# Kernel tuning notes

Hardware: AMD Instinct MI355X
Metric: run time of the kernel (lower is better)

The kernel has to match this reference:

```python
import jax, jax.numpy as jnp
import numpy as np

B, V, E = 32, 2048, 12288
IMG_F = 512
GCN_DIMS = [(3 + IMG_F, 512), (512, 512), (512, 512), (512, 512), (512, 64), (64, 3)]
FC_DIMS = [(V * 3, 1024), (1024, 1024), (1024, V * 3)]


def setup_inputs() -> dict:
    key = jax.random.key(0)
    ks = jax.random.split(key, 3 + len(GCN_DIMS) + len(FC_DIMS))
    inp = {}
    inp["vertices"] = jax.random.normal(ks[0], (B, V, 3), dtype=jnp.float32)
    inp["img_features"] = jax.random.normal(ks[1], (B, IMG_F), dtype=jnp.float32)
    inp["edge_index"] = jax.random.randint(ks[2], (2, E), 0, V, dtype=jnp.int32)
    for i, (fi, fo) in enumerate(GCN_DIMS):
        inp[f"W{i+1}"] = (jax.random.normal(ks[3 + i], (fi, fo), dtype=jnp.float32) / np.sqrt(fi)).astype(jnp.float32)
        inp[f"b{i+1}"] = jnp.zeros((fo,), dtype=jnp.float32)
    for i, (fi, fo) in enumerate(FC_DIMS):
        inp[f"fcW{i+1}"] = (jax.random.normal(ks[3 + len(GCN_DIMS) + i], (fi, fo), dtype=jnp.float32) / np.sqrt(fi)).astype(jnp.float32)
        inp[f"fcb{i+1}"] = jnp.zeros((fo,), dtype=jnp.float32)
    return inp


def _gcn_norm(edge_index):
    # PyG GCNConv: add self-loops, symmetric normalization 1/sqrt(d_i d_j).
    loop = jnp.arange(V, dtype=edge_index.dtype)
    src = jnp.concatenate([edge_index[0], loop])
    dst = jnp.concatenate([edge_index[1], loop])
    deg = jax.ops.segment_sum(jnp.ones_like(dst, dtype=jnp.float32), dst, num_segments=V)
    dinv = jax.lax.rsqrt(deg)  # deg >= 1 due to self-loops
    norm = dinv[src] * dinv[dst]  # [E+V]
    return src, dst, norm


def _gcn_layer(x, W, b, src, dst, norm):
    # x: [B, V, Fin] -> [B, V, Fout]; transform then gather/scatter aggregate.
    h = jnp.einsum("bvi,io->bvo", x, W)
    msg = h[:, src, :] * norm[None, :, None]          # gather over edges
    agg = jax.vmap(lambda m: jax.ops.segment_sum(m, dst, num_segments=V))(msg)
    return agg + b


def reference(vertices, img_features, edge_index,
              W1, b1, W2, b2, W3, b3, W4, b4, W5, b5, W6, b6,
              fcW1, fcb1, fcW2, fcb2, fcW3, fcb3):
    src, dst, norm = _gcn_norm(edge_index)
    # concat vertex coords with broadcast image feature: [B, V, 3+512]
    x = jnp.concatenate([vertices, jnp.broadcast_to(img_features[:, None, :], (B, V, IMG_F))], axis=2)
    x = _gcn_layer(x, W1, b1, src, dst, norm)
    x = _gcn_layer(x, W2, b2, src, dst, norm)
    x = jax.nn.relu(x)
    x = _gcn_layer(x, W3, b3, src, dst, norm)
    x = _gcn_layer(x, W4, b4, src, dst, norm)
    x = jax.nn.relu(x)
    x = _gcn_layer(x, W5, b5, src, dst, norm)
    x = _gcn_layer(x, W6, b6, src, dst, norm)
    x = jax.nn.relu(x)
    x = x.reshape(B, V * 3)
    h = x @ fcW1 + fcb1
    h = h @ fcW2 + fcb2
    h = jnp.tanh(h @ fcW3 + fcb3)
    deformations = h.reshape(B, V, 3) * 0.1
    return vertices + deformations
```

## Files before the change

kernel.cpp:

```cpp
#include <hip/hip_runtime.h>
#include <stdint.h>
#include <math.h>

#define B_ 32
#define V_ 2048
#define E_ 12288
#define M_ (B_*V_)

typedef __bf16 bf16x8 __attribute__((ext_vector_type(8)));
typedef float f32x4 __attribute__((ext_vector_type(4)));

__device__ __forceinline__ float bf2f(unsigned short u){
  union { unsigned int i; float f; } v; v.i = ((unsigned int)u) << 16; return v.f;
}
__device__ __forceinline__ unsigned short f2bf(float f){
  union { float f; unsigned int i; } v; v.f = f;
  unsigned int r = (v.i + 0x7fffu + ((v.i >> 16) & 1u)) >> 16;
  return (unsigned short)r;
}
__device__ __forceinline__ void gload16(const unsigned short* g, unsigned short* l){
  __builtin_amdgcn_global_load_lds(
      (const __attribute__((address_space(1))) void*)g,
      (__attribute__((address_space(3))) void*)l, 16, 0, 0);
}

__global__ __launch_bounds__(1024) void k_pre0(
    const int* __restrict__ ei, int* __restrict__ rowptr_g, int* __restrict__ cols_g,
    float* __restrict__ vals_g, float* __restrict__ selfw_g,
    float* __restrict__ wsum_g, float* __restrict__ w2_g,
    const float* __restrict__ W3, const float* __restrict__ W4,
    const float* __restrict__ img, const float* __restrict__ W1,
    unsigned short* __restrict__ W3B, unsigned short* __restrict__ W4T,
    float* __restrict__ partB){
  __shared__ int   sdeg[V_];
  __shared__ int   srp[V_ + 1];
  __shared__ int   sfill[V_];
  __shared__ float sdinv[V_];
  __shared__ float swsum[V_];
  __shared__ float sw2[V_];
  __shared__ int   swt[16];
  __shared__ __align__(16) float tile[4][32][33];
  if (blockIdx.x == 0){
    const int t = threadIdx.x;
    sdeg[2*t] = 0; sdeg[2*t+1] = 0; sfill[2*t] = 0; sfill[2*t+1] = 0;
    __syncthreads();
    #pragma unroll
    for (int e = t; e < E_; e += 1024) atomicAdd(&sdeg[ei[E_ + e]], 1);
    __syncthreads();
    int c0 = sdeg[2*t], c1 = sdeg[2*t+1];
    int s2 = c0 + c1;
    int lane = t & 63, wid = t >> 6;
    int pre = s2;
    #pragma unroll
    for (int off = 1; off < 64; off <<= 1){
      int u = __shfl_up(pre, off);
      if (lane >= off) pre += u;
    }
    if (lane == 63) swt[wid] = pre;
    __syncthreads();
    if (t == 0){
      int run = 0;
      #pragma unroll
      for (int i = 0; i < 16; i++){ int x = swt[i]; swt[i] = run; run += x; }
      srp[V_] = run;
    }
    __syncthreads();
    int base = swt[wid] + (pre - s2);
    srp[2*t] = base; srp[2*t+1] = base + c0;
    #pragma unroll
    for (int v = t; v < V_; v += 1024){
      float d = (float)(sdeg[v] + 1);
      float di = rsqrtf(d);
      sdinv[v] = di;
      swsum[v] = di * di;
    }
    __syncthreads();
    #pragma unroll
    for (int e = t; e < E_; e += 1024){
      int s = ei[e], d = ei[E_ + e];
      int pos = srp[d] + atomicAdd(&sfill[d], 1);
      float val = sdinv[s] * sdinv[d];
      cols_g[pos] = s;
      vals_g[pos] = val;
      atomicAdd(&swsum[d], val);
    }
    __syncthreads();
    #pragma unroll
    for (int v = t; v < V_; v += 1024)
      sw2[v] = (sdinv[v] * sdinv[v]) * swsum[v];
    __syncthreads();
    #pragma unroll
    for (int e = t; e < E_; e += 1024){
      int s = ei[e], d = ei[E_ + e];
      atomicAdd(&sw2[d], sdinv[s] * sdinv[d] * swsum[s]);
    }
    __syncthreads();
    #pragma unroll
    for (int v = t; v < V_; v += 1024){
      rowptr_g[v] = srp[v];
      selfw_g[v]  = sdinv[v] * sdinv[v];
      wsum_g[v]   = swsum[v];
      w2_g[v]     = sw2[v];
    }
    if (t == 0) rowptr_g[V_] = srp[V_];
  } else {
    int u = blockIdx.x - 1;
    int t10 = threadIdx.x;
    int sub = (u << 2) + (t10 >> 8);
    int t = t10 & 255;
    int ti = t10 >> 8;
    if (sub < 256){
      int tr0 = (sub >> 4) << 5, tc0 = (sub & 15) << 5;
      int r = t >> 5, c = t & 31;
      #pragma unroll
      for (int i = 0; i < 4; i++)
        tile[ti][r + 8*i][c] = W4[(size_t)(tr0 + r + 8*i) * 512 + tc0 + c];
      __syncthreads();
      #pragma unroll
      for (int i = 0; i < 4; i++)
        W4T[(size_t)(tc0 + r + 8*i) * 512 + tr0 + c] = f2bf(tile[ti][c][r + 8*i]);
    } else if (sub < 256 + 1024){
      int id = (sub - 256) * 256 + t;
      W3B[id] = f2bf(W3[id]);
    } else {
      int g = sub - 1280;
      int kc = g >> 1, nh = g & 1;
      int k0 = kc * 16;
      float* xs = &tile[ti][0][0];
      for (int i = t; i < 512; i += 256)
        xs[i] = img[(size_t)(i >> 4) * 512 + k0 + (i & 15)];
      __syncthreads();
      const float* W = W1 + 3 * 512;
      int n = (nh << 8) + t;
      float acc[32] = {};
      #pragma unroll
      for (int kg = 0; kg < 4; kg++){
        const float* wp = W + (size_t)(k0 + kg * 4) * 512 + n;
        float w0 = wp[0], w1 = wp[512], w2 = wp[1024], w3 = wp[1536];
        #pragma unroll
        for (int r = 0; r < 32; r++){
          f32x4 xv = *(const f32x4*)&xs[r * 16 + kg * 4];
          acc[r] += xv[0]*w0 + xv[1]*w1 + xv[2]*w2 + xv[3]*w3;
        }
      }
      float* p = partB + (size_t)kc * 16384 + n;
      #pragma unroll
      for (int r = 0; r < 32; r++) p[(size_t)r * 512] = acc[r];
    }
  }
}

__global__ __launch_bounds__(256) void k_preB(
    const float* __restrict__ partB, float* __restrict__ I1,
    const float* __restrict__ b3, const float* __restrict__ W4,
    const float* __restrict__ W5, const float* __restrict__ W6,
    const float* __restrict__ b5,
    float* __restrict__ C34, float* __restrict__ W56, float* __restrict__ C56){
  int blk = blockIdx.x, t = threadIdx.x;
  if (blk < 64){
    int id = blk * 256 + t;
    float a = 0.f;
    #pragma unroll
    for (int s = 0; s < 32; s++) a += partB[(size_t)s * 16384 + id];
    I1[id] = a;
  } else {
    int id = (blk - 64) * 256 + t;
    if (id < 512){
      float a0=0,a1=0,a2=0,a3=0;
      for (int k = 0; k < 512; k += 4){
        a0 += b3[k]   * W4[(size_t)k * 512 + id];
        a1 += b3[k+1] * W4[(size_t)(k+1) * 512 + id];
        a2 += b3[k+2] * W4[(size_t)(k+2) * 512 + id];
        a3 += b3[k+3] * W4[(size_t)(k+3) * 512 + id];
      }
      C34[id] = a0+a1+a2+a3;
    } else if (id < 512 + 1536){
      int i = id - 512; int k5 = i / 3, j = i % 3;
      float a = 0.f;
      #pragma unroll 4
      for (int u = 0; u < 64; u++) a += W5[k5 * 64 + u] * W6[u * 3 + j];
      W56[i] = a;
    } else if (id < 512 + 1536 + 3){
      int j = id - (512 + 1536);
      float a = 0.f;
      #pragma unroll 4
      for (int u = 0; u < 64; u++) a += b5[u] * W6[u * 3 + j];
      C56[j] = a;
    }
  }
}

__global__ __launch_bounds__(256) void k_preC(
    const float* __restrict__ b1, const float* __restrict__ W1,
    const float* __restrict__ I1, const float* __restrict__ W2,
    float* __restrict__ partB){
  __shared__ __align__(16) float xs[36 * 16];
  int g = blockIdx.x;
  int kc = g >> 1, k0 = kc * 16;
  int t = threadIdx.x;
  int n = ((g & 1) << 8) + t;
  for (int i = t; i < 576; i += 256){
    int r = i >> 4, kk = i & 15;
    const float* q;
    if (r == 0)      q = b1;
    else if (r < 4)  q = W1 + (size_t)(r - 1) * 512;
    else             q = I1 + (size_t)(r - 4) * 512;
    xs[i] = q[k0 + kk];
  }
  __syncthreads();
  float acc[36] = {};
  #pragma unroll
  for (int kg = 0; kg < 4; kg++){
    const float* wp = W2 + (size_t)(k0 + kg * 4) * 512 + n;
    float w0 = wp[0], w1 = wp[512], w2 = wp[1024], w3 = wp[1536];
    #pragma unroll
    for (int r = 0; r < 36; r++){
      f32x4 xv = *(const f32x4*)&xs[r * 16 + kg * 4];
      acc[r] += xv[0]*w0 + xv[1]*w1 + xv[2]*w2 + xv[3]*w3;
    }
  }
  float* p = partB + (size_t)kc * 18432 + n;
  #pragma unroll
  for (int r = 0; r < 36; r++) p[(size_t)r * 512] = acc[r];
}

__global__ __launch_bounds__(256) void k_preD(
    const float* __restrict__ partB, float* __restrict__ P){
  int id = blockIdx.x * 256 + threadIdx.x;
  float a = 0.f;
  #pragma unroll
  for (int s = 0; s < 32; s++) a += partB[(size_t)s * 18432 + id];
  P[id] = a;
}

__global__ __launch_bounds__(1024) void k_va2(
    const float* __restrict__ in, const int* __restrict__ rowptr,
    const int* __restrict__ cols, const float* __restrict__ vals,
    const float* __restrict__ selfw, float* __restrict__ outv){
  __shared__ float xs[V_ * 3];
  __shared__ float ys[V_ * 3];
  int b = blockIdx.x, t = threadIdx.x;
  const float* ib = in + (size_t)b * V_ * 3;
  for (int i = t; i < V_ * 3; i += 1024) xs[i] = ib[i];
  __syncthreads();
  for (int v = t; v < V_; v += 1024){
    float sw = selfw[v];
    float a0 = sw * xs[v*3], a1 = sw * xs[v*3+1], a2 = sw * xs[v*3+2];
    int re = rowptr[v + 1];
    for (int e = rowptr[v]; e < re; e++){
      int s = cols[e]; float vv = vals[e];
      a0 += vv * xs[s*3]; a1 += vv * xs[s*3+1]; a2 += vv * xs[s*3+2];
    }
    ys[v*3] = a0; ys[v*3+1] = a1; ys[v*3+2] = a2;
  }
  __syncthreads();
  for (int v = t; v < V_; v += 1024){
    float sw = selfw[v];
    float a0 = sw * ys[v*3], a1 = sw * ys[v*3+1], a2 = sw * ys[v*3+2];
    int re = rowptr[v + 1];
    for (int e = rowptr[v]; e < re; e++){
      int s = cols[e]; float vv = vals[e];
      a0 += vv * ys[s*3]; a1 += vv * ys[s*3+1]; a2 += vv * ys[s*3+2];
    }
    float* o = outv + ((size_t)v * 32 + b) * 3;
    o[0] = a0; o[1] = a1; o[2] = a2;
  }
}

__global__ __launch_bounds__(1024) void k_x2(
    const float* __restrict__ va2v, const float* __restrict__ P,
    const float* __restrict__ wsum, const float* __restrict__ w2s,
    const float* __restrict__ b2,
    unsigned short* __restrict__ Y){
  int v = (blockIdx.x << 2) + (threadIdx.x >> 8);
  int batch = (blockIdx.y << 2) + ((threadIdx.x >> 6) & 3);
  int f8 = (threadIdx.x & 63) * 8;
  const float* va = va2v + ((size_t)v * 32 + batch) * 3;
  float x0 = va[0], x1 = va[1], x2 = va[2];
  float w2v = w2s[v], wsv = wsum[v];
  float tt[8];
  #pragma unroll
  for (int h = 0; h < 2; h++){
    f32x4 wv0 = *(const f32x4*)&P[512  + f8 + 4*h];
    f32x4 wv1 = *(const f32x4*)&P[1024 + f8 + 4*h];
    f32x4 wv2 = *(const f32x4*)&P[1536 + f8 + 4*h];
    f32x4 ccv = *(const f32x4*)&P[f8 + 4*h];
    f32x4 bbv = *(const f32x4*)&b2[f8 + 4*h];
    f32x4 iiv = *(const f32x4*)&P[2048 + (size_t)batch * 512 + f8 + 4*h];
    #pragma unroll
    for (int j = 0; j < 4; j++){
      float tv = x0*wv0[j] + x1*wv1[j] + x2*wv2[j] + w2v*iiv[j] + wsv*ccv[j] + bbv[j];
      tt[4*h + j] = fmaxf(tv, 0.f);
    }
  }
  unsigned int o[4];
  #pragma unroll
  for (int i = 0; i < 4; i++)
    o[i] = (unsigned int)f2bf(tt[2*i]) | ((unsigned int)f2bf(tt[2*i+1]) << 16);
  *(uint4*)&Y[((size_t)v * 32 + batch) * 512 + f8] = *(uint4*)o;
}

__global__ __launch_bounds__(128) void k_aggv(
    const unsigned short* __restrict__ Hg, const int* __restrict__ rowptr,
    const int* __restrict__ cols, const float* __restrict__ vals,
    const float* __restrict__ selfw, unsigned short* __restrict__ Xo){
  int bid = blockIdx.x;
  int bg  = bid & 7;
  int dst = (bid >> 3) & (V_ - 1);
  int fc  = bid >> 14;
  int t = threadIdx.x;
  int batch = (bg << 2) + (t >> 5);
  int f8 = (fc << 8) + (t & 31) * 8;
  int rs = rowptr[dst], re = rowptr[dst + 1];
  float sw = selfw[dst];
  float a[8];
  {
    uint4 q = *(const uint4*)&Hg[((size_t)dst * 32 + batch) * 512 + f8];
    const unsigned int* w = (const unsigned int*)&q;
    #pragma unroll
    for (int i = 0; i < 4; i++){
      a[2*i]   = sw * bf2f(w[i] & 0xffff);
      a[2*i+1] = sw * bf2f(w[i] >> 16);
    }
  }
  int e = rs;
  for (; e + 1 < re; e += 2){
    int s0 = cols[e], s1 = cols[e+1];
    float v0 = vals[e], v1 = vals[e+1];
    uint4 q0 = *(const uint4*)&Hg[((size_t)s0 * 32 + batch) * 512 + f8];
    uint4 q1 = *(const uint4*)&Hg[((size_t)s1 * 32 + batch) * 512 + f8];
    const unsigned int* w0 = (const unsigned int*)&q0;
    const unsigned int* w1 = (const unsigned int*)&q1;
    #pragma unroll
    for (int i = 0; i < 4; i++){
      a[2*i]   += v0 * bf2f(w0[i] & 0xffff) + v1 * bf2f(w1[i] & 0xffff);
      a[2*i+1] += v0 * bf2f(w0[i] >> 16)    + v1 * bf2f(w1[i] >> 16);
    }
  }
  if (e < re){
    int s = cols[e]; float v = vals[e];
    uint4 q = *(const uint4*)&Hg[((size_t)s * 32 + batch) * 512 + f8];
    const unsigned int* w = (const unsigned int*)&q;
    #pragma unroll
    for (int i = 0; i < 4; i++){
      a[2*i]   += v * bf2f(w[i] & 0xffff);
      a[2*i+1] += v * bf2f(w[i] >> 16);
    }
  }
  unsigned int o[4];
  #pragma unroll
  for (int i = 0; i < 4; i++)
    o[i] = (unsigned int)f2bf(a[2*i]) | ((unsigned int)f2bf(a[2*i+1]) << 16);
  *(uint4*)&Xo[((size_t)dst * 32 + batch) * 512 + f8] = *(uint4*)o;
}

template<int BM, int BN, int WM, int WN, int TM, int TN>
__global__ __launch_bounds__(WM*WN*64) void k_gemm(
    const unsigned short* __restrict__ Xg, const unsigned short* __restrict__ Wt,
    unsigned short* __restrict__ Hg, int K, int N,
    const float* __restrict__ wsumv, const float* __restrict__ cvec,
    const float* __restrict__ bias, int relu,
    const float* __restrict__ W56g, float* __restrict__ h5p){
  constexpr int BK = 32;
  constexpr int NW = WM * WN;
  constexpr int NT = NW * 64;
  constexpr int RA = BM / NW;
  constexpr int RB = BN / NW;
  __shared__ __align__(16) unsigned short As[2][BM * BK];
  __shared__ __align__(16) unsigned short Bs[2][BN * BK];
  __shared__ float h5s[BM * 3];
  const int tid = threadIdx.x;
  const int row0 = blockIdx.x * BM, col0 = blockIdx.y * BN;
  const int wave = tid >> 6, lane = tid & 63;
  const int wr = wave / WN, wc = wave % WN;
  const int lrow = lane & 15, lq = lane >> 4;
  const int lrw = lane >> 2, lcol = (lane & 3) * 8;
  const int arow = wave * RA, brow = wave * RB;
  if (h5p){
    for (int i = tid; i < BM * 3; i += NT) h5s[i] = 0.f;
  }
  f32x4 acc[TM][TN] = {};
  #pragma unroll
  for (int t = 0; t < RA / 16; t++)
    gload16(&Xg[(size_t)(row0 + arow + t * 16 + lrw) * K + lcol],
            &As[0][(arow + t * 16) * BK]);
  #pragma unroll
  for (int t = 0; t < RB / 16; t++)
    gload16(&Wt[(size_t)(col0 + brow + t * 16 + lrw) * K + lcol],
            &Bs[0][(brow + t * 16) * BK]);
  int cur = 0;
  for (int k0 = 0; k0 < K; k0 += BK){
    __syncthreads();
    if (k0 + BK < K){
      #pragma unroll
      for (int t = 0; t < RA / 16; t++)
        gload16(&Xg[(size_t)(row0 + arow + t * 16 + lrw) * K + k0 + BK + lcol],
                &As[cur ^ 1][(arow + t * 16) * BK]);
      #pragma unroll
      for (int t = 0; t < RB / 16; t++)
        gload16(&Wt[(size_t)(col0 + brow + t * 16 + lrw) * K + k0 + BK + lcol],
                &Bs[cur ^ 1][(brow + t * 16) * BK]);
    }
    bf16x8 af[TM], bfr[TN];
    #pragma unroll
    for (int tm = 0; tm < TM; tm++)
      af[tm] = *(const bf16x8*)&As[cur][(wr * TM * 16 + tm * 16 + lrow) * BK + lq * 8];
    #pragma unroll
    for (int tn = 0; tn < TN; tn++)
      bfr[tn] = *(const bf16x8*)&Bs[cur][(wc * TN * 16 + tn * 16 + lrow) * BK + lq * 8];
    #pragma unroll
    for (int tm = 0; tm < TM; tm++)
      #pragma unroll
      for (int tn = 0; tn < TN; tn++)
        acc[tm][tn] = __builtin_amdgcn_mfma_f32_16x16x32_bf16(af[tm], bfr[tn], acc[tm][tn], 0, 0, 0);
    cur ^= 1;
  }
  if (h5p){
    float w56l[TN][3], cvl[TN], bvl[TN];
    #pragma unroll
    for (int tn = 0; tn < TN; tn++){
      int col = col0 + wc * TN * 16 + tn * 16 + lrow;
      cvl[tn] = cvec[col]; bvl[tn] = bias[col];
      w56l[tn][0] = W56g[col * 3];
      w56l[tn][1] = W56g[col * 3 + 1];
      w56l[tn][2] = W56g[col * 3 + 2];
    }
    #pragma unroll
    for (int tm = 0; tm < TM; tm++){
      #pragma unroll
      for (int r = 0; r < 4; r++){
        int lr = wr * TM * 16 + tm * 16 + lq * 4 + r;
        float ws = wsumv[(row0 + lr) >> 5];
        float p0 = 0.f, p1 = 0.f, p2 = 0.f;
        #pragma unroll
        for (int tn = 0; tn < TN; tn++){
          float x = fmaxf(acc[tm][tn][r] + ws * cvl[tn] + bvl[tn], 0.f);
          p0 += x * w56l[tn][0]; p1 += x * w56l[tn][1]; p2 += x * w56l[tn][2];
        }
        #pragma unroll
        for (int off = 8; off; off >>= 1){
          p0 += __shfl_down(p0, off);
          p1 += __shfl_down(p1, off);
          p2 += __shfl_down(p2, off);
        }
        if (lrow == 0){
          atomicAdd(&h5s[lr * 3 + 0], p0);
          atomicAdd(&h5s[lr * 3 + 1], p1);
          atomicAdd(&h5s[lr * 3 + 2], p2);
        }
      }
    }
    __syncthreads();
    float* dst = h5p + (size_t)blockIdx.y * ((size_t)M_ * 3) + (size_t)row0 * 3;
    for (int i = tid; i < BM * 3; i += NT) dst[i] = h5s[i];
  } else {
    #pragma unroll
    for (int tm = 0; tm < TM; tm++){
      #pragma unroll
      for (int tn = 0; tn < TN; tn++){
        int col = col0 + wc * TN * 16 + tn * 16 + lrow;
        float cv = 0.f, bv = 0.f;
        if (cvec){ cv = cvec[col]; bv = bias[col]; }
        #pragma unroll
        for (int r = 0; r < 4; r++){
          int row = row0 + wr * TM * 16 + tm * 16 + lq * 4 + r;
          float x = acc[tm][tn][r];
          if (cvec) x += wsumv[row >> 5] * cv + bv;
          if (relu) x = fmaxf(x, 0.f);
          Hg[(size_t)row * N + col] = f2bf(x);
        }
      }
    }
  }
}

__global__ __launch_bounds__(1024) void k_xa2(
    const float* __restrict__ h5p, const int* __restrict__ rowptr,
    const int* __restrict__ cols, const float* __restrict__ vals,
    const float* __restrict__ selfw, const float* __restrict__ wsum,
    const float* __restrict__ C56, const float* __restrict__ b6,
    float* __restrict__ XF){
  __shared__ float xs[V_ * 3];
  __shared__ float ys[V_ * 3];
  int b = blockIdx.x, t = threadIdx.x;
  const size_t M3 = (size_t)M_ * 3;
  for (int i = t; i < V_ * 3; i += 1024){
    int v = i / 3, j = i - v * 3;
    size_t g = ((size_t)v * 32 + b) * 3 + j;
    xs[i] = h5p[g] + h5p[M3 + g] + h5p[2 * M3 + g] + h5p[3 * M3 + g];
  }
  __syncthreads();
  for (int v = t; v < V_; v += 1024){
    float sw = selfw[v];
    float a0 = sw * xs[v*3], a1 = sw * xs[v*3+1], a2 = sw * xs[v*3+2];
    int re = rowptr[v + 1];
    for (int e = rowptr[v]; e < re; e++){
      int s = cols[e]; float vv = vals[e];
      a0 += vv * xs[s*3]; a1 += vv * xs[s*3+1]; a2 += vv * xs[s*3+2];
    }
    ys[v*3] = a0; ys[v*3+1] = a1; ys[v*3+2] = a2;
  }
  __syncthreads();
  float* ob = XF + (size_t)b * V_ * 3;
  for (int v = t; v < V_; v += 1024){
    float sw = selfw[v];
    float a0 = sw * ys[v*3], a1 = sw * ys[v*3+1], a2 = sw * ys[v*3+2];
    int re = rowptr[v + 1];
    for (int e = rowptr[v]; e < re; e++){
      int s = cols[e]; float vv = vals[e];
      a0 += vv * ys[s*3]; a1 += vv * ys[s*3+1]; a2 += vv * ys[s*3+2];
    }
    float w = wsum[v];
    a0 = fmaxf(a0 + w * C56[0] + b6[0], 0.f);
    a1 = fmaxf(a1 + w * C56[1] + b6[1], 0.f);
    a2 = fmaxf(a2 + w * C56[2] + b6[2], 0.f);
    ob[v*3] = a0; ob[v*3+1] = a1; ob[v*3+2] = a2;
  }
}

template<int R, int KC>
__global__ __launch_bounds__(256) void k_fcp(
    const float* __restrict__ in, const float* __restrict__ W,
    float* __restrict__ partial, int K, int N){
  const int n = blockIdx.x * 256 + threadIdx.x;
  const int k0 = blockIdx.y * KC;
  float acc[R] = {};
  for (int kk = 0; kk < KC; kk += 4){
    const float* wp = W + (size_t)(k0 + kk) * N + n;
    float w0 = wp[0];
    float w1 = wp[(size_t)N];
    float w2 = wp[(size_t)2 * N];
    float w3 = wp[(size_t)3 * N];
    #pragma unroll
    for (int r = 0; r < R; r++){
      const float* xp = in + (size_t)r * K + k0 + kk;
      acc[r] += xp[0]*w0 + xp[1]*w1 + xp[2]*w2 + xp[3]*w3;
    }
  }
  float* p = partial + (size_t)blockIdx.y * R * N + n;
  #pragma unroll
  for (int r = 0; r < R; r++) p[(size_t)r * N] = acc[r];
}

__global__ __launch_bounds__(256) void k_fcr(
    const float* __restrict__ partial, const float* __restrict__ bias,
    float* __restrict__ out, int total, int N, int KS, int mode,
    const float* __restrict__ vert){
  int id = blockIdx.x * 256 + threadIdx.x;
  if (id >= total) return;
  int n = id % N;
  float a0 = 0.f, a1 = 0.f, a2 = 0.f, a3 = 0.f;
  int s = 0;
  for (; s + 4 <= KS; s += 4){
    a0 += partial[(size_t)s * total + id];
    a1 += partial[(size_t)(s + 1) * total + id];
    a2 += partial[(size_t)(s + 2) * total + id];
    a3 += partial[(size_t)(s + 3) * total + id];
  }
  for (; s < KS; s++) a0 += partial[(size_t)s * total + id];
  float acc = a0 + a1 + a2 + a3;
  if (bias) acc += bias[n];
  if (mode) acc = vert[id] + 0.1f * tanhf(acc);
  out[id] = acc;
}

static constexpr size_t AL(size_t x){ return (x + 255) & ~(size_t)255; }
static constexpr size_t S512 = (size_t)M_ * 512 * 2;
static constexpr size_t S3   = (size_t)M_ * 3 * 4;
static constexpr size_t OXA  = 0;
static constexpr size_t OXB  = OXA  + AL(S512);
static constexpr size_t OVA2 = OXB  + AL(S512);
static constexpr size_t OH5P = OVA2 + AL(S3);
static constexpr size_t OXF  = OH5P + AL(4 * S3);
static constexpr size_t OFC1 = OXF  + AL(S3);
static constexpr size_t OFC2 = OFC1 + AL((size_t)B_ * 1024 * 4);
static constexpr size_t OI1  = OFC2 + AL((size_t)B_ * 1024 * 4);
static constexpr size_t OP   = OI1  + AL((size_t)32 * 512 * 4);
static constexpr size_t OC34 = OP   + AL((size_t)36 * 512 * 4);
static constexpr size_t OW56 = OC34 + AL((size_t)512 * 4);
static constexpr size_t OC56 = OW56 + AL((size_t)512 * 3 * 4);
static constexpr size_t OW3B = OC56 + AL((size_t)3 * 4);
static constexpr size_t OW4T = OW3B + AL((size_t)512 * 512 * 2);
static constexpr size_t OW34 = OW4T + AL((size_t)512 * 512 * 2);
static constexpr size_t OROW = OW34 + AL((size_t)512 * 512 * 2);
static constexpr size_t OCOL = OROW + AL((size_t)(V_ + 1) * 4);
static constexpr size_t OVAL = OCOL + AL((size_t)E_ * 4);
static constexpr size_t OSELF= OVAL + AL((size_t)E_ * 4);
static constexpr size_t OWS  = OSELF+ AL((size_t)V_ * 4);
static constexpr size_t OW2S = OWS  + AL((size_t)V_ * 4);

extern "C" void kernel_launch(void* const* d_in, const int* in_sizes, int n_in,
                              void* d_out, int out_size, void* d_ws, size_t ws_size,
                              hipStream_t stream){
  const float* vert  = (const float*)d_in[0];
  const float* img   = (const float*)d_in[1];
  const int*   ei    = (const int*)  d_in[2];
  const float* W1 = (const float*)d_in[3],  *b1 = (const float*)d_in[4];
  const float* W2 = (const float*)d_in[5],  *b2 = (const float*)d_in[6];
  const float* W3 = (const float*)d_in[7],  *b3 = (const float*)d_in[8];
  const float* W4 = (const float*)d_in[9],  *b4 = (const float*)d_in[10];
  const float* W5 = (const float*)d_in[11], *b5 = (const float*)d_in[12];
  const float* W6 = (const float*)d_in[13], *b6 = (const float*)d_in[14];
  const float* fcW1 = (const float*)d_in[15], *fcb1 = (const float*)d_in[16];
  const float* fcW2 = (const float*)d_in[17], *fcb2 = (const float*)d_in[18];
  const float* fcW3 = (const float*)d_in[19], *fcb3 = (const float*)d_in[20];
  float* out = (float*)d_out;

  char* ws = (char*)d_ws;
  unsigned short* XA  = (unsigned short*)(ws + OXA);
  unsigned short* XB  = (unsigned short*)(ws + OXB);
  float* VA2v = (float*)(ws + OVA2);
  float* H5P  = (float*)(ws + OH5P);
  float* XF   = (float*)(ws + OXF);
  float* FC1o = (float*)(ws + OFC1);
  float* FC2o = (float*)(ws + OFC2);
  float* I1   = (float*)(ws + OI1);
  float* P    = (float*)(ws + OP);
  float* C34  = (float*)(ws + OC34);
  float* W56  = (float*)(ws + OW56);
  float* C56  = (float*)(ws + OC56);
  unsigned short* W3B = (unsigned short*)(ws + OW3B);
  unsigned short* W4T = (unsigned short*)(ws + OW4T);
  unsigned short* W34 = (unsigned short*)(ws + OW34);
  float* PARTA = (float*)(ws + OXA);
  float* PARTB = (float*)(ws + OXB);
  int*   ROW  = (int*)(ws + OROW);
  int*   COL  = (int*)(ws + OCOL);
  float* VAL  = (float*)(ws + OVAL);
  float* SELF = (float*)(ws + OSELF);
  float* WSUM = (float*)(ws + OWS);
  float* W2S  = (float*)(ws + OW2S);

  k_pre0<<<337, 1024, 0, stream>>>(ei, ROW, COL, VAL, SELF, WSUM, W2S,
                                   W3, W4, img, W1, W3B, W4T, PARTB);
  k_preB<<<64 + 9, 256, 0, stream>>>(PARTB, I1, b3, W4, W5, W6, b5, C34, W56, C56);
  k_preC<<<64, 256, 0, stream>>>(b1, W1, I1, W2, PARTB);
  k_preD<<<72, 256, 0, stream>>>(PARTB, P);
  k_gemm<64,64,2,2,2,2><<<dim3(8, 8), 256, 0, stream>>>(W4T, W3B, W34, 512, 512,
                                                        nullptr, nullptr, nullptr, 0,
                                                        nullptr, nullptr);

  k_va2<<<B_, 1024, 0, stream>>>(vert, ROW, COL, VAL, SELF, VA2v);
  k_x2<<<dim3(V_ / 4, 8), 1024, 0, stream>>>(VA2v, P, WSUM, W2S, b2, XA);
  k_aggv<<<V_ * 16, 128, 0, stream>>>(XA, ROW, COL, VAL, SELF, XB);
  k_aggv<<<V_ * 16, 128, 0, stream>>>(XB, ROW, COL, VAL, SELF, XA);

  k_gemm<128,128,2,2,4,4><<<dim3(M_ / 128, 4), 256, 0, stream>>>(XA, W34, XB, 512, 512,
                                                                 WSUM, C34, b4, 1,
                                                                 W56, H5P);

  k_xa2<<<B_, 1024, 0, stream>>>(H5P, ROW, COL, VAL, SELF, WSUM, C56, b6, XF);

  k_fcp<32,64><<<dim3(4, 96), 256, 0, stream>>>(XF, fcW1, PARTA, 6144, 1024);
  k_fcr<<<(B_ * 1024 + 255) / 256, 256, 0, stream>>>(PARTA, fcb1, FC1o, 32 * 1024, 1024, 96, 0, nullptr);
  k_fcp<32,64><<<dim3(4, 16), 256, 0, stream>>>(FC1o, fcW2, PARTA, 1024, 1024);
  k_fcr<<<(B_ * 1024 + 255) / 256, 256, 0, stream>>>(PARTA, fcb2, FC2o, 32 * 1024, 1024, 16, 0, nullptr);
  k_fcp<32,64><<<dim3(24, 16), 256, 0, stream>>>(FC2o, fcW3, PARTA, 1024, 6144);
  k_fcr<<<(B_ * 6144 + 255) / 256, 256, 0, stream>>>(PARTA, fcb3, out, 32 * 6144, 6144, 16, 1, vert);
}
```

Before: 539.7 us.

## Loop N tiles inside GEMM block and regroup aggregation blocks by vertex

After: 559.9 us. 3.7% more time.

```diff
diff --git a/kernel.cpp b/kernel.cpp
--- a/kernel.cpp
+++ b/kernel.cpp
@@ -9,6 +9,7 @@
 
 typedef __bf16 bf16x8 __attribute__((ext_vector_type(8)));
 typedef float f32x4 __attribute__((ext_vector_type(4)));
+typedef unsigned int u32x4 __attribute__((ext_vector_type(4)));
 
 __device__ __forceinline__ float bf2f(unsigned short u){
   union { unsigned int i; float f; } v; v.i = ((unsigned int)u) << 16; return v.f;
@@ -300,17 +301,20 @@
   *(uint4*)&Y[((size_t)v * 32 + batch) * 512 + f8] = *(uint4*)o;
 }
 
-__global__ __launch_bounds__(128) void k_aggv(
+__global__ __launch_bounds__(256) void k_aggv(
     const unsigned short* __restrict__ Hg, const int* __restrict__ rowptr,
     const int* __restrict__ cols, const float* __restrict__ vals,
     const float* __restrict__ selfw, unsigned short* __restrict__ Xo){
   int bid = blockIdx.x;
-  int bg  = bid & 7;
-  int dst = (bid >> 3) & (V_ - 1);
-  int fc  = bid >> 14;
+  int bgLo = bid & 7;
+  int dstB = (bid >> 3) & 511;
+  int bgHi = (bid >> 12) & 1;
+  int fc   = bid >> 13;
   int t = threadIdx.x;
-  int batch = (bg << 2) + (t >> 5);
-  int f8 = (fc << 8) + (t & 31) * 8;
+  int wave = t >> 6, lane = t & 63;
+  int dst = dstB * 4 + wave;
+  int batch = bgHi * 16 + bgLo * 2 + (lane >> 5);
+  int f8 = fc * 256 + (lane & 31) * 8;
   int rs = rowptr[dst], re = rowptr[dst + 1];
   float sw = selfw[dst];
   float a[8];
@@ -347,14 +351,14 @@
       a[2*i+1] += v * bf2f(w[i] >> 16);
     }
   }
-  unsigned int o[4];
+  u32x4 o;
   #pragma unroll
   for (int i = 0; i < 4; i++)
     o[i] = (unsigned int)f2bf(a[2*i]) | ((unsigned int)f2bf(a[2*i+1]) << 16);
-  *(uint4*)&Xo[((size_t)dst * 32 + batch) * 512 + f8] = *(uint4*)o;
-}
-
-template<int BM, int BN, int WM, int WN, int TM, int TN>
+  __builtin_nontemporal_store(o, (u32x4*)&Xo[((size_t)dst * 32 + batch) * 512 + f8]);
+}
+
+template<int BM, int BN, int WM, int WN, int TM, int TN, int NL>
 __global__ __launch_bounds__(WM*WN*64) void k_gemm(
     const unsigned short* __restrict__ Xg, const unsigned short* __restrict__ Wt,
     unsigned short* __restrict__ Hg, int K, int N,
@@ -370,7 +374,8 @@
   __shared__ __align__(16) unsigned short Bs[2][BN * BK];
   __shared__ float h5s[BM * 3];
   const int tid = threadIdx.x;
-  const int row0 = blockIdx.x * BM, col0 = blockIdx.y * BN;
+  const int row0 = blockIdx.x * BM;
+  const int colB0 = blockIdx.y * BN * NL;
   const int wave = tid >> 6, lane = tid & 63;
   const int wr = wave / WN, wc = wave % WN;
   const int lrow = lane & 15, lq = lane >> 4;
@@ -386,91 +391,104 @@
             &As[0][(arow + t * 16) * BK]);
   #pragma unroll
   for (int t = 0; t < RB / 16; t++)
-    gload16(&Wt[(size_t)(col0 + brow + t * 16 + lrw) * K + lcol],
+    gload16(&Wt[(size_t)(colB0 + brow + t * 16 + lrw) * K + lcol],
             &Bs[0][(brow + t * 16) * BK]);
   int cur = 0;
-  for (int k0 = 0; k0 < K; k0 += BK){
-    __syncthreads();
-    if (k0 + BK < K){
-      #pragma unroll
-      for (int t = 0; t < RA / 16; t++)
-        gload16(&Xg[(size_t)(row0 + arow + t * 16 + lrw) * K + k0 + BK + lcol],
-                &As[cur ^ 1][(arow + t * 16) * BK]);
-      #pragma unroll
-      for (int t = 0; t < RB / 16; t++)
-        gload16(&Wt[(size_t)(col0 + brow + t * 16 + lrw) * K + k0 + BK + lcol],
-                &Bs[cur ^ 1][(brow + t * 16) * BK]);
-    }
-    bf16x8 af[TM], bfr[TN];
-    #pragma unroll
-    for (int tm = 0; tm < TM; tm++)
-      af[tm] = *(const bf16x8*)&As[cur][(wr * TM * 16 + tm * 16 + lrow) * BK + lq * 8];
-    #pragma unroll
-    for (int tn = 0; tn < TN; tn++)
-      bfr[tn] = *(const bf16x8*)&Bs[cur][(wc * TN * 16 + tn * 16 + lrow) * BK + lq * 8];
-    #pragma unroll
-    for (int tm = 0; tm < TM; tm++)
+  for (int nt = 0; nt < NL; nt++){
+    const int col0 = colB0 + nt * BN;
+    for (int k0 = 0; k0 < K; k0 += BK){
+      __syncthreads();
+      int k2 = k0 + BK, nt2 = nt;
+      if (k2 >= K){ k2 = 0; nt2 = nt + 1; }
+      if (nt2 < NL){
+        #pragma unroll
+        for (int t = 0; t < RA / 16; t++)
+          gload16(&Xg[(size_t)(row0 + arow + t * 16 + lrw) * K + k2 + lcol],
+                  &As[cur ^ 1][(arow + t * 16) * BK]);
+        #pragma unroll
+        for (int t = 0; t < RB / 16; t++)
+          gload16(&Wt[(size_t)(colB0 + nt2 * BN + brow + t * 16 + lrw) * K + k2 + lcol],
+                  &Bs[cur ^ 1][(brow + t * 16) * BK]);
+      }
+      bf16x8 af[TM], bfr[TN];
+      #pragma unroll
+      for (int tm = 0; tm < TM; tm++)
+        af[tm] = *(const bf16x8*)&As[cur][(wr * TM * 16 + tm * 16 + lrow) * BK + lq * 8];
       #pragma unroll
       for (int tn = 0; tn < TN; tn++)
-        acc[tm][tn] = __builtin_amdgcn_mfma_f32_16x16x32_bf16(af[tm], bfr[tn], acc[tm][tn], 0, 0, 0);
-    cur ^= 1;
-  }
-  if (h5p){
-    float w56l[TN][3], cvl[TN], bvl[TN];
-    #pragma unroll
-    for (int tn = 0; tn < TN; tn++){
-      int col = col0 + wc * TN * 16 + tn * 16 + lrow;
-      cvl[tn] = cvec[col]; bvl[tn] = bias[col];
-      w56l[tn][0] = W56g[col * 3];
-      w56l[tn][1] = W56g[col * 3 + 1];
-      w56l[tn][2] = W56g[col * 3 + 2];
-    }
-    #pragma unroll
-    for (int tm = 0; tm < TM; tm++){
-      #pragma unroll
-      for (int r = 0; r < 4; r++){
-        int lr = wr * TM * 16 + tm * 16 + lq * 4 + r;
-        float ws = wsumv[(row0 + lr) >> 5];
-        float p0 = 0.f, p1 = 0.f, p2 = 0.f;
+        bfr[tn] = *(const bf16x8*)&Bs[cur][(wc * TN * 16 + tn * 16 + lrow) * BK + lq * 8];
+      #pragma unroll
+      for (int tm = 0; tm < TM; tm++)
+        #pragma unroll
+        for (int tn = 0; tn < TN; tn++)
+          acc[tm][tn] = __builtin_amdgcn_mfma_f32_16x16x32_bf16(af[tm], bfr[tn], acc[tm][tn], 0, 0, 0);
+      cur ^= 1;
+    }
+    if (h5p){
+      float w56l[TN][3], cvl[TN], bvl[TN];
+      #pragma unroll
+      for (int tn = 0; tn < TN; tn++){
+        int col = col0 + wc * TN * 16 + tn * 16 + lrow;
+        cvl[tn] = cvec[col]; bvl[tn] = bias[col];
+        w56l[tn][0] = W56g[col * 3];
+        w56l[tn][1] = W56g[col * 3 + 1];
+        w56l[tn][2] = W56g[col * 3 + 2];
+      }
+      #pragma unroll
+      for (int tm = 0; tm < TM; tm++){
+        #pragma unroll
+        for (int r = 0; r < 4; r++){
+          int lr = wr * TM * 16 + tm * 16 + lq * 4 + r;
+          float ws = wsumv[(row0 + lr) >> 5];
+          float p0 = 0.f, p1 = 0.f, p2 = 0.f;
+          #pragma unroll
+          for (int tn = 0; tn < TN; tn++){
+            float x = fmaxf(acc[tm][tn][r] + ws * cvl[tn] + bvl[tn], 0.f);
+            p0 += x * w56l[tn][0]; p1 += x * w56l[tn][1]; p2 += x * w56l[tn][2];
+          }
+          #pragma unroll
+          for (int off = 8; off; off >>= 1){
+            p0 += __shfl_down(p0, off);
+            p1 += __shfl_down(p1, off);
+            p2 += __shfl_down(p2, off);
+          }
+          if (lrow == 0){
+            atomicAdd(&h5s[lr * 3 + 0], p0);
+            atomicAdd(&h5s[lr * 3 + 1], p1);
+            atomicAdd(&h5s[lr * 3 + 2], p2);
+          }
+        }
+      }
+      #pragma unroll
+      for (int tm = 0; tm < TM; tm++)
+        #pragma unroll
+        for (int tn = 0; tn < TN; tn++)
+          acc[tm][tn] = (f32x4){0.f, 0.f, 0.f, 0.f};
+    } else {
+      #pragma unroll
+      for (int tm = 0; tm < TM; tm++){
         #pragma unroll
         for (int tn = 0; tn < TN; tn++){
-          float x = fmaxf(acc[tm][tn][r] + ws * cvl[tn] + bvl[tn], 0.f);
-          p0 += x * w56l[tn][0]; p1 += x * w56l[tn][1]; p2 += x * w56l[tn][2];
-        }
-        #pragma unroll
-        for (int off = 8; off; off >>= 1){
-          p0 += __shfl_down(p0, off);
-          p1 += __shfl_down(p1, off);
-          p2 += __shfl_down(p2, off);
-        }
-        if (lrow == 0){
-          atomicAdd(&h5s[lr * 3 + 0], p0);
-          atomicAdd(&h5s[lr * 3 + 1], p1);
-          atomicAdd(&h5s[lr * 3 + 2], p2);
+          int col = col0 + wc * TN * 16 + tn * 16 + lrow;
+          float cv = 0.f, bv = 0.f;
+          if (cvec){ cv = cvec[col]; bv = bias[col]; }
+          #pragma unroll
+          for (int r = 0; r < 4; r++){
+            int row = row0 + wr * TM * 16 + tm * 16 + lq * 4 + r;
+            float x = acc[tm][tn][r];
+            if (cvec) x += wsumv[row >> 5] * cv + bv;
+            if (relu) x = fmaxf(x, 0.f);
+            Hg[(size_t)row * N + col] = f2bf(x);
+          }
+          acc[tm][tn] = (f32x4){0.f, 0.f, 0.f, 0.f};
         }
       }
     }
+  }
+  if (h5p){
     __syncthreads();
     float* dst = h5p + (size_t)blockIdx.y * ((size_t)M_ * 3) + (size_t)row0 * 3;
     for (int i = tid; i < BM * 3; i += NT) dst[i] = h5s[i];
-  } else {
-    #pragma unroll
-    for (int tm = 0; tm < TM; tm++){
-      #pragma unroll
-      for (int tn = 0; tn < TN; tn++){
-        int col = col0 + wc * TN * 16 + tn * 16 + lrow;
-        float cv = 0.f, bv = 0.f;
-        if (cvec){ cv = cvec[col]; bv = bias[col]; }
-        #pragma unroll
-        for (int r = 0; r < 4; r++){
-          int row = row0 + wr * TM * 16 + tm * 16 + lq * 4 + r;
-          float x = acc[tm][tn][r];
-          if (cvec) x += wsumv[row >> 5] * cv + bv;
-          if (relu) x = fmaxf(x, 0.f);
-          Hg[(size_t)row * N + col] = f2bf(x);
-        }
-      }
-    }
   }
 }
 
@@ -483,11 +501,9 @@
   __shared__ float xs[V_ * 3];
   __shared__ float ys[V_ * 3];
   int b = blockIdx.x, t = threadIdx.x;
-  const size_t M3 = (size_t)M_ * 3;
   for (int i = t; i < V_ * 3; i += 1024){
     int v = i / 3, j = i - v * 3;
-    size_t g = ((size_t)v * 32 + b) * 3 + j;
-    xs[i] = h5p[g] + h5p[M3 + g] + h5p[2 * M3 + g] + h5p[3 * M3 + g];
+    xs[i] = h5p[((size_t)v * 32 + b) * 3 + j];
   }
   __syncthreads();
   for (int v = t; v < V_; v += 1024){
@@ -636,18 +652,18 @@
   k_preB<<<64 + 9, 256, 0, stream>>>(PARTB, I1, b3, W4, W5, W6, b5, C34, W56, C56);
   k_preC<<<64, 256, 0, stream>>>(b1, W1, I1, W2, PARTB);
   k_preD<<<72, 256, 0, stream>>>(PARTB, P);
-  k_gemm<64,64,2,2,2,2><<<dim3(8, 8), 256, 0, stream>>>(W4T, W3B, W34, 512, 512,
-                                                        nullptr, nullptr, nullptr, 0,
-                                                        nullptr, nullptr);
+  k_gemm<64,64,2,2,2,2,1><<<dim3(8, 8), 256, 0, stream>>>(W4T, W3B, W34, 512, 512,
+                                                          nullptr, nullptr, nullptr, 0,
+                                                          nullptr, nullptr);
 
   k_va2<<<B_, 1024, 0, stream>>>(vert, ROW, COL, VAL, SELF, VA2v);
   k_x2<<<dim3(V_ / 4, 8), 1024, 0, stream>>>(VA2v, P, WSUM, W2S, b2, XA);
-  k_aggv<<<V_ * 16, 128, 0, stream>>>(XA, ROW, COL, VAL, SELF, XB);
-  k_aggv<<<V_ * 16, 128, 0, stream>>>(XB, ROW, COL, VAL, SELF, XA);
-
-  k_gemm<128,128,2,2,4,4><<<dim3(M_ / 128, 4), 256, 0, stream>>>(XA, W34, XB, 512, 512,
-                                                                 WSUM, C34, b4, 1,
-                                                                 W56, H5P);
+  k_aggv<<<16384, 256, 0, stream>>>(XA, ROW, COL, VAL, SELF, XB);
+  k_aggv<<<16384, 256, 0, stream>>>(XB, ROW, COL, VAL, SELF, XA);
+
+  k_gemm<128,128,2,2,4,4,4><<<dim3(M_ / 128, 1), 256, 0, stream>>>(XA, W34, XB, 512, 512,
+                                                                   WSUM, C34, b4, 1,
+                                                                   W56, H5P);
 
   k_xa2<<<B_, 1024, 0, stream>>>(H5P, ROW, COL, VAL, SELF, WSUM, C56, b6, XF);
 
```
